# Kernel tuning notes

Measured on AMD Instinct MI355X. Metric: run time of the kernel, lower is better.

Reference implementation:

```python
import jax, jax.numpy as jnp
import numpy as np

N = 50000          # nodes
E = 800000         # edges (before self-loops)
D_IN, D_H, D_OUT = 128, 256, 256
SZ_C = 2           # channels
NUM_GRAPHS = 64
EPS = 1e-6


def setup_inputs() -> dict:
    key = jax.random.key(0)
    ks = jax.random.split(key, 12)
    x = jax.random.normal(ks[0], (N, D_IN), dtype=jnp.float32)
    edge = jax.random.randint(ks[1], (2, E), 0, N, dtype=jnp.int64)
    batch = jnp.sort(jax.random.randint(ks[2], (N,), 0, NUM_GRAPHS, dtype=jnp.int64))
    def glorot(k, shape):
        fan = shape[-2] + shape[-1]
        return jax.random.normal(k, shape, dtype=jnp.float32) * jnp.sqrt(2.0 / fan)
    W0 = glorot(ks[3], (SZ_C, D_IN, D_H)); b0 = jnp.zeros((SZ_C, D_H), jnp.float32)
    W1 = glorot(ks[4], (SZ_C, D_H, D_H));  b1 = jnp.zeros((SZ_C, D_H), jnp.float32)
    W2 = glorot(ks[5], (SZ_C, D_H, D_OUT)); b2 = jnp.zeros((SZ_C, D_OUT), jnp.float32)
    ln_w = jnp.ones((D_OUT,), jnp.float32)
    ln_b = jnp.zeros((D_OUT,), jnp.float32)
    return {"x": x, "edge": edge, "batch": batch,
            "W0": W0, "b0": b0, "W1": W1, "b1": b1, "W2": W2, "b2": b2,
            "ln_w": ln_w, "ln_b": ln_b}


def _gcn_conv(h, W, b, src, dst, norm):
    # PyG GCNConv: linear transform, then deg-normalized scatter-add, then bias
    h = h @ W                                  # [N, d_out]
    msg = h[src] * norm[:, None]               # [E+N, d_out] gathered messages
    agg = jax.ops.segment_sum(msg, dst, num_segments=N)
    return agg + b


def reference(x, edge, batch, W0, b0, W1, b1, W2, b2, ln_w, ln_b):
    # add self-loops (GCNConv default add_self_loops=True)
    loops = jnp.arange(N, dtype=edge.dtype)
    src = jnp.concatenate([edge[0], loops])
    dst = jnp.concatenate([edge[1], loops])
    # symmetric normalization: deg^{-1/2}[src] * deg^{-1/2}[dst], deg over targets
    deg = jax.ops.segment_sum(jnp.ones_like(dst, dtype=x.dtype), dst, num_segments=N)
    dinv = jnp.where(deg > 0, jax.lax.rsqrt(deg), 0.0)
    norm = dinv[src] * dinv[dst]

    channels = []
    for c in range(SZ_C):  # small fixed channel count
        h = x
        for (W, b) in ((W0[c], b0[c]), (W1[c], b1[c]), (W2[c], b2[c])):
            h = _gcn_conv(h, W, b, src, dst, norm)
            h = jax.nn.relu(h) + h  # residual: ReLU output + pre-ReLU input
        channels.append(h)
    channal = jnp.stack(channels)              # [sz_c, N, d_out]

    mean = channal.mean(-1, keepdims=True)
    var = channal.var(-1, keepdims=True)
    out = (channal - mean) * jax.lax.rsqrt(var + EPS) * ln_w + ln_b

    batchs = jnp.ones((SZ_C, 1), channal.dtype) * batch.astype(channal.dtype)[None, :]
    return out, batchs
```

## Files before the change

kernel.cpp:

```cpp
#include <hip/hip_runtime.h>
#include <hip/hip_bf16.h>

typedef __bf16 v8bf __attribute__((ext_vector_type(8)));
typedef float  v4f  __attribute__((ext_vector_type(4)));

constexpr int N_NODES = 50000;
constexpr int N_EDGES = 800000;
constexpr float LN_EPS = 1e-6f;
constexpr int ROW_TILES = N_NODES / 16;

__global__ void probe_kernel(const int* __restrict__ edge, int* __restrict__ flag) {
  int t = threadIdx.x;
  int nz = 0;
  for (int i = t * 2 + 1; i < 4096; i += 128) nz |= (edge[i] != 0);
  unsigned long long m = __ballot(nz);
  if (t == 0) flag[0] = (m == 0ull) ? 1 : 0;
}

__device__ __forceinline__ int ld_idx(const void* base, int i, int is64) {
  int v;
  if (is64) v = (int)((const long long*)base)[(long long)i];
  else      v = ((const int*)base)[i];
  if ((unsigned)v >= (unsigned)N_NODES) v = 0;
  return v;
}


__global__ void init_kernel(int* __restrict__ deg, int* __restrict__ gcount) {
  int i = blockIdx.x * 256 + threadIdx.x;
  if (i < N_NODES) deg[i] = 1;
  if (i == 0) gcount[0] = 0;
}

__global__ void count_kernel(const void* __restrict__ edge, const int* __restrict__ flag,
                             int* __restrict__ deg) {
  int e = blockIdx.x * 256 + threadIdx.x;
  if (e < N_EDGES) atomicAdd(&deg[ld_idx(edge, N_EDGES + e, flag[0])], 1);
}

__global__ __launch_bounds__(256) void block_offsets_kernel(
    const int* __restrict__ deg, int* __restrict__ gcount,
    int* __restrict__ rowstart, int* __restrict__ cursor, float* __restrict__ dinv) {
  __shared__ int ps[256];
  __shared__ int base_s;
  int tid = threadIdx.x;
  int node = blockIdx.x * 256 + tid;
  int d = (node < N_NODES) ? deg[node] : 1;
  int cnt = d - 1;
  ps[tid] = cnt;
  __syncthreads();
#pragma unroll
  for (int off = 1; off < 256; off <<= 1) {
    int v = (tid >= off) ? ps[tid - off] : 0;
    __syncthreads();
    ps[tid] += v;
    __syncthreads();
  }
  if (tid == 255) base_s = atomicAdd(gcount, ps[255]);
  __syncthreads();
  int start = base_s + ps[tid] - cnt;
  if (node < N_NODES) {
    rowstart[node] = start;
    cursor[node]   = start;
    dinv[node]     = rsqrtf((float)max(d, 1));
  }
}

__global__ void scatter_kernel(const void* __restrict__ edge, const int* __restrict__ flag,
                               int* __restrict__ cursor, int* __restrict__ csr_src) {
  int e = blockIdx.x * 256 + threadIdx.x;
  if (e >= N_EDGES) return;
  int f = flag[0];
  int s = ld_idx(edge, e, f);
  int d = ld_idx(edge, N_EDGES + e, f);
  int pos = atomicAdd(&cursor[d], 1);
  if ((unsigned)pos < (unsigned)N_EDGES) csr_src[pos] = s;
}

__global__ void pack_all_kernel(const float* __restrict__ W0, const float* __restrict__ W1,
                                const float* __restrict__ W2, __bf16* __restrict__ Wp) {
  int tid = blockIdx.x * 256 + threadIdx.x;
  const float* src; int local;
  if (tid < 65536)       { src = W0 + (size_t)(tid >> 15) * (128 * 256); local = tid & 32767; }
  else if (tid < 196608) { int t2 = tid - 65536;  src = W1 + (size_t)(t2 >> 16) * 65536; local = t2 & 65535; }
  else                   { int t2 = tid - 196608; src = W2 + (size_t)(t2 >> 16) * 65536; local = t2 & 65535; }
  int j    = local & 7;
  int lane = (local >> 3) & 63;
  int ct   = (local >> 9) & 15;
  int kc   = local >> 13;
  int k    = kc * 32 + ((lane >> 4) << 3) + j;
  int col  = ct * 16 + (lane & 15);
  Wp[tid] = (__bf16)src[k * 256 + col];
}

__global__ __launch_bounds__(256) void prescale_x_kernel(
    const float* __restrict__ x, const float* __restrict__ dinv, __bf16* __restrict__ xd) {
  int t = blockIdx.x * 256 + threadIdx.x;
  int node = t >> 4;
  int d0 = (t & 15) * 8;
  float di = dinv[node];
  v4f f0 = *(const v4f*)(x + (size_t)node * 128 + d0);
  v4f f1 = *(const v4f*)(x + (size_t)node * 128 + d0 + 4);
  v8bf o;
#pragma unroll
  for (int j = 0; j < 4; j++) { o[j] = (__bf16)(di * f0[j]); o[4 + j] = (__bf16)(di * f1[j]); }
  *(v8bf*)(xd + (size_t)node * 128 + d0) = o;
}

__global__ __launch_bounds__(256) void agg128_kernel(
    const __bf16* __restrict__ Yd, const int* __restrict__ rowstart,
    const int* __restrict__ deg, const int* __restrict__ csr_src,
    const float* __restrict__ dinv, __bf16* __restrict__ U) {
  int node = blockIdx.x * 4 + (threadIdx.x >> 6);
  int lane = threadIdx.x & 63;
  int sub = lane >> 4;
  int d0 = (lane & 15) * 8;

  int start = rowstart[node];
  int cnt = deg[node] - 1;
  start = max(0, min(start, N_EDGES));
  cnt = max(0, min(cnt, N_EDGES - start));
  int e = start, end = start + cnt;

  float di = dinv[node];
  v8bf ys = *(const v8bf*)(Yd + (unsigned)(node * 128 + d0));

  float a[8];
#pragma unroll
  for (int j = 0; j < 8; j++) a[j] = 0.f;

  for (; e + 16 <= end; e += 16) {
    int s0 = csr_src[e + sub];
    int s1 = csr_src[e + 4 + sub];
    int s2 = csr_src[e + 8 + sub];
    int s3 = csr_src[e + 12 + sub];
    if ((unsigned)s0 >= (unsigned)N_NODES) s0 = 0;
    if ((unsigned)s1 >= (unsigned)N_NODES) s1 = 0;
    if ((unsigned)s2 >= (unsigned)N_NODES) s2 = 0;
    if ((unsigned)s3 >= (unsigned)N_NODES) s3 = 0;
    v8bf y0 = *(const v8bf*)(Yd + (unsigned)(s0 * 128 + d0));
    v8bf y1 = *(const v8bf*)(Yd + (unsigned)(s1 * 128 + d0));
    v8bf y2 = *(const v8bf*)(Yd + (unsigned)(s2 * 128 + d0));
    v8bf y3 = *(const v8bf*)(Yd + (unsigned)(s3 * 128 + d0));
#pragma unroll
    for (int j = 0; j < 8; j++)
      a[j] += ((float)y0[j] + (float)y1[j]) + ((float)y2[j] + (float)y3[j]);
  }
  if (e + 8 <= end) {
    int s0 = csr_src[e + sub];
    int s1 = csr_src[e + 4 + sub];
    if ((unsigned)s0 >= (unsigned)N_NODES) s0 = 0;
    if ((unsigned)s1 >= (unsigned)N_NODES) s1 = 0;
    v8bf y0 = *(const v8bf*)(Yd + (unsigned)(s0 * 128 + d0));
    v8bf y1 = *(const v8bf*)(Yd + (unsigned)(s1 * 128 + d0));
#pragma unroll
    for (int j = 0; j < 8; j++) a[j] += (float)y0[j] + (float)y1[j];
    e += 8;
  }
  if (e + 4 <= end) {
    int s0 = csr_src[e + sub];
    if ((unsigned)s0 >= (unsigned)N_NODES) s0 = 0;
    v8bf y0 = *(const v8bf*)(Yd + (unsigned)(s0 * 128 + d0));
#pragma unroll
    for (int j = 0; j < 8; j++) a[j] += (float)y0[j];
    e += 4;
  }
  int rem = end - e;
  if (sub < rem) {
    int s0 = csr_src[e + sub];
    if ((unsigned)s0 >= (unsigned)N_NODES) s0 = 0;
    v8bf y0 = *(const v8bf*)(Yd + (unsigned)(s0 * 128 + d0));
#pragma unroll
    for (int j = 0; j < 8; j++) a[j] += (float)y0[j];
  }

#pragma unroll
  for (int off = 16; off < 64; off <<= 1)
#pragma unroll
    for (int j = 0; j < 8; j++) a[j] += __shfl_xor(a[j], off);

  if (sub == 0) {
    v8bf u;
#pragma unroll
    for (int j = 0; j < 8; j++) u[j] = (__bf16)(di * (a[j] + (float)ys[j]));
    *(v8bf*)(U + (unsigned)(node * 128 + d0)) = u;
  }
}

__global__ __launch_bounds__(256) void agg_fused512_kernel(
    const __bf16* __restrict__ A,
    const int* __restrict__ rowstart, const int* __restrict__ deg,
    const int* __restrict__ csr_src, const float* __restrict__ dinv,
    __bf16* __restrict__ U) {
  int node = blockIdx.x * 4 + (threadIdx.x >> 6);
  int lane = threadIdx.x & 63;
  int d0 = lane * 8;

  int start = rowstart[node];
  int cnt = deg[node] - 1;
  start = max(0, min(start, N_EDGES));
  cnt = max(0, min(cnt, N_EDGES - start));
  int e = start, end = start + cnt;

  float di = dinv[node];
  v8bf ys = *(const v8bf*)(A + (unsigned)(node * 512 + d0));

  float a[8];
#pragma unroll
  for (int j = 0; j < 8; j++) a[j] = 0.f;

  for (; e + 8 <= end; e += 8) {
    int s0 = csr_src[e],     s1 = csr_src[e + 1];
    int s2 = csr_src[e + 2], s3 = csr_src[e + 3];
    int s4 = csr_src[e + 4], s5 = csr_src[e + 5];
    int s6 = csr_src[e + 6], s7 = csr_src[e + 7];
    if ((unsigned)s0 >= (unsigned)N_NODES) s0 = 0;
    if ((unsigned)s1 >= (unsigned)N_NODES) s1 = 0;
    if ((unsigned)s2 >= (unsigned)N_NODES) s2 = 0;
    if ((unsigned)s3 >= (unsigned)N_NODES) s3 = 0;
    if ((unsigned)s4 >= (unsigned)N_NODES) s4 = 0;
    if ((unsigned)s5 >= (unsigned)N_NODES) s5 = 0;
    if ((unsigned)s6 >= (unsigned)N_NODES) s6 = 0;
    if ((unsigned)s7 >= (unsigned)N_NODES) s7 = 0;
    v8bf y0 = *(const v8bf*)(A + (unsigned)(s0 * 512 + d0));
    v8bf y1 = *(const v8bf*)(A + (unsigned)(s1 * 512 + d0));
    v8bf y2 = *(const v8bf*)(A + (unsigned)(s2 * 512 + d0));
    v8bf y3 = *(const v8bf*)(A + (unsigned)(s3 * 512 + d0));
    v8bf y4 = *(const v8bf*)(A + (unsigned)(s4 * 512 + d0));
    v8bf y5 = *(const v8bf*)(A + (unsigned)(s5 * 512 + d0));
    v8bf y6 = *(const v8bf*)(A + (unsigned)(s6 * 512 + d0));
    v8bf y7 = *(const v8bf*)(A + (unsigned)(s7 * 512 + d0));
#pragma unroll
    for (int j = 0; j < 8; j++)
      a[j] += (((float)y0[j] + (float)y1[j]) + ((float)y2[j] + (float)y3[j])) +
              (((float)y4[j] + (float)y5[j]) + ((float)y6[j] + (float)y7[j]));
  }
  if (e + 4 <= end) {
    int s0 = csr_src[e],     s1 = csr_src[e + 1];
    int s2 = csr_src[e + 2], s3 = csr_src[e + 3];
    if ((unsigned)s0 >= (unsigned)N_NODES) s0 = 0;
    if ((unsigned)s1 >= (unsigned)N_NODES) s1 = 0;
    if ((unsigned)s2 >= (unsigned)N_NODES) s2 = 0;
    if ((unsigned)s3 >= (unsigned)N_NODES) s3 = 0;
    v8bf y0 = *(const v8bf*)(A + (unsigned)(s0 * 512 + d0));
    v8bf y1 = *(const v8bf*)(A + (unsigned)(s1 * 512 + d0));
    v8bf y2 = *(const v8bf*)(A + (unsigned)(s2 * 512 + d0));
    v8bf y3 = *(const v8bf*)(A + (unsigned)(s3 * 512 + d0));
#pragma unroll
    for (int j = 0; j < 8; j++)
      a[j] += ((float)y0[j] + (float)y1[j]) + ((float)y2[j] + (float)y3[j]);
    e += 4;
  }
  for (; e < end; e++) {
    int s0 = csr_src[e];
    if ((unsigned)s0 >= (unsigned)N_NODES) s0 = 0;
    v8bf y0 = *(const v8bf*)(A + (unsigned)(s0 * 512 + d0));
#pragma unroll
    for (int j = 0; j < 8; j++) a[j] += (float)y0[j];
  }

  v8bf u;
#pragma unroll
  for (int j = 0; j < 8; j++) u[j] = (__bf16)(di * (a[j] + (float)ys[j]));
  *(v8bf*)(U + (unsigned)(node * 512 + d0)) = u;
}

template <int K, int LDA, int LDO>
__global__ __launch_bounds__(256, 2) void gemm_mid_kernel(
    const __bf16* __restrict__ A, const __bf16* __restrict__ Wp,
    const float* __restrict__ bias, const float* __restrict__ dinv,
    __bf16* __restrict__ Hd) {
  constexpr int KC = K / 32;
  int lane = threadIdx.x & 63;
  int wave = threadIdx.x >> 6;

  v8bf bfrag[KC][4];
#pragma unroll
  for (int kc = 0; kc < KC; kc++)
#pragma unroll
    for (int c4 = 0; c4 < 4; c4++)
      bfrag[kc][c4] = *(const v8bf*)(Wp + ((size_t)((kc * 16 + wave * 4 + c4) * 64 + lane)) * 8);

  int arow = lane & 15;
  int akq = (lane >> 4) * 8;
  int ccol = wave * 64 + (lane & 15);
  float bcol[4];
#pragma unroll
  for (int c4 = 0; c4 < 4; c4++) bcol[c4] = bias[ccol + c4 * 16];

  for (int t = blockIdx.x; t < ROW_TILES; t += gridDim.x) {
    int row0 = t * 16;
    const __bf16* Ap = A + (size_t)(row0 + arow) * LDA + akq;
    v8bf af[KC];
#pragma unroll
    for (int kc = 0; kc < KC; kc++) af[kc] = *(const v8bf*)(Ap + kc * 32);

    v4f acc[4];
#pragma unroll
    for (int c4 = 0; c4 < 4; c4++) acc[c4] = (v4f){0.f, 0.f, 0.f, 0.f};
#pragma unroll
    for (int kc = 0; kc < KC; kc++)
#pragma unroll
      for (int c4 = 0; c4 < 4; c4++)
        acc[c4] = __builtin_amdgcn_mfma_f32_16x16x32_bf16(af[kc], bfrag[kc][c4], acc[c4], 0, 0, 0);

    int crow = row0 + ((lane >> 4) << 2);
    float dv[4];
#pragma unroll
    for (int r = 0; r < 4; r++) dv[r] = dinv[crow + r];
#pragma unroll
    for (int c4 = 0; c4 < 4; c4++)
#pragma unroll
      for (int r = 0; r < 4; r++) {
        float z = acc[c4][r] + bcol[c4];
        float h = z + fmaxf(z, 0.f);
        Hd[(size_t)(crow + r) * LDO + ccol + c4 * 16] = (__bf16)(dv[r] * h);
      }
  }
}

__global__ __launch_bounds__(256, 2) void gemm_final_kernel(
    const __bf16* __restrict__ A, const __bf16* __restrict__ Wp,
    const float* __restrict__ bias, const float* __restrict__ lnw,
    const float* __restrict__ lnb, float* __restrict__ out) {
  constexpr int KC = 8;
  constexpr int LDA = 512;
  __shared__ float ls1[4][16];
  __shared__ float ls2[4][16];
  int lane = threadIdx.x & 63;
  int wave = threadIdx.x >> 6;

  v8bf bfrag[KC][4];
#pragma unroll
  for (int kc = 0; kc < KC; kc++)
#pragma unroll
    for (int c4 = 0; c4 < 4; c4++)
      bfrag[kc][c4] = *(const v8bf*)(Wp + ((size_t)((kc * 16 + wave * 4 + c4) * 64 + lane)) * 8);

  int arow = lane & 15;
  int akq = (lane >> 4) * 8;
  int g = lane >> 4;
  int ccol = wave * 64 + (lane & 15);
  float bcol[4], wcol[4], lbcol[4];
#pragma unroll
  for (int c4 = 0; c4 < 4; c4++) {
    int col = ccol + c4 * 16;
    bcol[c4] = bias[col];
    wcol[c4] = lnw[col];
    lbcol[c4] = lnb[col];
  }

  for (int t = blockIdx.x; t < ROW_TILES; t += gridDim.x) {
    int row0 = t * 16;
    const __bf16* Ap = A + (size_t)(row0 + arow) * LDA + akq;
    v8bf af[KC];
#pragma unroll
    for (int kc = 0; kc < KC; kc++) af[kc] = *(const v8bf*)(Ap + kc * 32);

    v4f acc[4];
#pragma unroll
    for (int c4 = 0; c4 < 4; c4++) acc[c4] = (v4f){0.f, 0.f, 0.f, 0.f};
#pragma unroll
    for (int kc = 0; kc < KC; kc++)
#pragma unroll
      for (int c4 = 0; c4 < 4; c4++)
        acc[c4] = __builtin_amdgcn_mfma_f32_16x16x32_bf16(af[kc], bfrag[kc][c4], acc[c4], 0, 0, 0);

    float h[4][4];
#pragma unroll
    for (int c4 = 0; c4 < 4; c4++)
#pragma unroll
      for (int r = 0; r < 4; r++) {
        float z = acc[c4][r] + bcol[c4];
        h[c4][r] = z + fmaxf(z, 0.f);
      }

    float s1[4], s2[4];
#pragma unroll
    for (int r = 0; r < 4; r++) {
      s1[r] = 0.f; s2[r] = 0.f;
#pragma unroll
      for (int c4 = 0; c4 < 4; c4++) { s1[r] += h[c4][r]; s2[r] += h[c4][r] * h[c4][r]; }
    }
#pragma unroll
    for (int off = 1; off < 16; off <<= 1)
#pragma unroll
      for (int r = 0; r < 4; r++) {
        s1[r] += __shfl_xor(s1[r], off);
        s2[r] += __shfl_xor(s2[r], off);
      }
    if ((lane & 15) == 0) {
#pragma unroll
      for (int r = 0; r < 4; r++) { ls1[wave][g * 4 + r] = s1[r]; ls2[wave][g * 4 + r] = s2[r]; }
    }
    __syncthreads();
#pragma unroll
    for (int r = 0; r < 4; r++) {
      int row = g * 4 + r;
      float t1 = ls1[0][row] + ls1[1][row] + ls1[2][row] + ls1[3][row];
      float t2 = ls2[0][row] + ls2[1][row] + ls2[2][row] + ls2[3][row];
      float mean = t1 * (1.0f / 256.0f);
      float var = t2 * (1.0f / 256.0f) - mean * mean;
      float rstd = rsqrtf(fmaxf(var, 0.f) + LN_EPS);
#pragma unroll
      for (int c4 = 0; c4 < 4; c4++)
        out[(size_t)(row0 + row) * 256 + ccol + c4 * 16] =
            (h[c4][r] - mean) * rstd * wcol[c4] + lbcol[c4];
    }
    __syncthreads();
  }
}

__global__ void batchs_kernel(const void* __restrict__ batch, const int* __restrict__ flag,
                              float* __restrict__ ob) {
  int i = blockIdx.x * 256 + threadIdx.x;
  if (i >= N_NODES) return;
  int f = flag[0];
  int v;
  if (f) v = (int)((const long long*)batch)[i];
  else   v = ((const int*)batch)[i];
  float b = (float)v;
  ob[i] = b;
  ob[N_NODES + i] = b;
}


extern "C" void kernel_launch(void* const* d_in, const int* in_sizes, int n_in,
                              void* d_out, int out_size, void* d_ws, size_t ws_size,
                              hipStream_t stream) {
  const float* x    = (const float*)d_in[0];
  const void*  edge = d_in[1];
  const void*  batch= d_in[2];
  const float* W0   = (const float*)d_in[3];
  const float* b0   = (const float*)d_in[4];
  const float* W1   = (const float*)d_in[5];
  const float* b1   = (const float*)d_in[6];
  const float* W2   = (const float*)d_in[7];
  const float* b2   = (const float*)d_in[8];
  const float* lnw  = (const float*)d_in[9];
  const float* lnb  = (const float*)d_in[10];

  float* out_x = (float*)d_out;
  float* out_b = (float*)d_out + (size_t)2 * N_NODES * 256;

  __bf16* UC  = (__bf16*)out_x;
  __bf16* HdC = (__bf16*)(out_x + (size_t)N_NODES * 256);

  char* p = (char*)d_ws;
  __bf16* Ubuf  = (__bf16*)p;  p += (size_t)N_NODES * 256 * 2;
  __bf16* xd    = Ubuf;
  __bf16* U0    = Ubuf + (size_t)N_NODES * 128;
  int* csr_src  = (int*)p;     p += (size_t)N_EDGES * 4;
  int* deg      = (int*)p;     p += (size_t)N_NODES * 4;
  int* cursor   = (int*)p;     p += (size_t)N_NODES * 4;
  int* rowstart = (int*)p;     p += (size_t)N_NODES * 4;
  float* dinv   = (float*)p;   p += (size_t)N_NODES * 4;
  int* flag     = (int*)p;     p += 16;
  int* gcount   = (int*)p;     p += 16;
  __bf16* Wp    = (__bf16*)p;

  const int EB = (N_EDGES + 255) / 256;
  const int NB = (N_NODES + 255) / 256;

  probe_kernel<<<1, 64, 0, stream>>>((const int*)edge, flag);
  init_kernel<<<NB, 256, 0, stream>>>(deg, gcount);
  count_kernel<<<EB, 256, 0, stream>>>(edge, flag, deg);
  block_offsets_kernel<<<NB, 256, 0, stream>>>(deg, gcount, rowstart, cursor, dinv);
  scatter_kernel<<<EB, 256, 0, stream>>>(edge, flag, cursor, csr_src);

  pack_all_kernel<<<1280, 256, 0, stream>>>(W0, W1, W2, Wp);

  prescale_x_kernel<<<3125, 256, 0, stream>>>(x, dinv, xd);
  agg128_kernel<<<N_NODES / 4, 256, 0, stream>>>(xd, rowstart, deg, csr_src, dinv, U0);

  gemm_mid_kernel<128, 128, 512><<<512, 256, 0, stream>>>(U0, Wp, b0, dinv, HdC);
  gemm_mid_kernel<128, 128, 512><<<512, 256, 0, stream>>>(U0, Wp + 32768, b0 + 256, dinv,
                                                          HdC + 256);

  agg_fused512_kernel<<<N_NODES / 4, 256, 0, stream>>>(HdC, rowstart, deg, csr_src, dinv, UC);
  gemm_mid_kernel<256, 512, 512><<<512, 256, 0, stream>>>(UC, Wp + 65536, b1, dinv, HdC);
  gemm_mid_kernel<256, 512, 512><<<512, 256, 0, stream>>>(UC + 256, Wp + 131072, b1 + 256,
                                                          dinv, HdC + 256);

  agg_fused512_kernel<<<N_NODES / 4, 256, 0, stream>>>(HdC, rowstart, deg, csr_src, dinv, UC);
  gemm_final_kernel<<<512, 256, 0, stream>>>(UC + 256, Wp + 262144, b2 + 256, lnw, lnb,
                                             out_x + (size_t)N_NODES * 256);
  gemm_final_kernel<<<512, 256, 0, stream>>>(UC, Wp + 196608, b2, lnw, lnb, out_x);

  batchs_kernel<<<NB, 256, 0, stream>>>(batch, flag, out_b);
}
```

Before: 622.4 us.

## Fuse neighbor aggregation with following GEMM for first two GCN layers

Replaces the separate aggregation and dual-channel GEMM kernels of layers 0 and 1 with fused kernels. Each block aggregates 16 nodes into an XOR-swizzled LDS tile, then runs MFMA for both channels and writes the prescaled residual-ReLU output directly. This removes the global write and reread of the aggregated intermediate and four launches. In exchange, each block streams the full weight fragments from L2 rather than keeping them in registers across a persistent loop. The output buffers are also re-aliased and the final GEMM launch order swapped to match.

After: 595.4 us. 1.05x faster.

```diff
diff --git a/kernel.cpp b/kernel.cpp
--- a/kernel.cpp
+++ b/kernel.cpp
@@ -107,91 +107,268 @@
   *(v8bf*)(xd + (size_t)node * 128 + d0) = o;
 }
 
-__global__ __launch_bounds__(256) void agg128_kernel(
+__global__ __launch_bounds__(256) void fused0_kernel(
     const __bf16* __restrict__ Yd, const int* __restrict__ rowstart,
     const int* __restrict__ deg, const int* __restrict__ csr_src,
-    const float* __restrict__ dinv, __bf16* __restrict__ U) {
-  int node = blockIdx.x * 4 + (threadIdx.x >> 6);
+    const float* __restrict__ dinv, const __bf16* __restrict__ Wp,
+    const float* __restrict__ bias,
+    __bf16* __restrict__ Hd) {
+  __shared__ __bf16 lds[16 * 128];
+  char* lb = (char*)lds;
+  int wave = threadIdx.x >> 6;
   int lane = threadIdx.x & 63;
   int sub = lane >> 4;
-  int d0 = (lane & 15) * 8;
-
-  int start = rowstart[node];
-  int cnt = deg[node] - 1;
-  start = max(0, min(start, N_EDGES));
-  cnt = max(0, min(cnt, N_EDGES - start));
-  int e = start, end = start + cnt;
-
-  float di = dinv[node];
-  v8bf ys = *(const v8bf*)(Yd + (unsigned)(node * 128 + d0));
-
-  float a[8];
-#pragma unroll
-  for (int j = 0; j < 8; j++) a[j] = 0.f;
-
-  for (; e + 16 <= end; e += 16) {
-    int s0 = csr_src[e + sub];
-    int s1 = csr_src[e + 4 + sub];
-    int s2 = csr_src[e + 8 + sub];
-    int s3 = csr_src[e + 12 + sub];
-    if ((unsigned)s0 >= (unsigned)N_NODES) s0 = 0;
-    if ((unsigned)s1 >= (unsigned)N_NODES) s1 = 0;
-    if ((unsigned)s2 >= (unsigned)N_NODES) s2 = 0;
-    if ((unsigned)s3 >= (unsigned)N_NODES) s3 = 0;
-    v8bf y0 = *(const v8bf*)(Yd + (unsigned)(s0 * 128 + d0));
-    v8bf y1 = *(const v8bf*)(Yd + (unsigned)(s1 * 128 + d0));
-    v8bf y2 = *(const v8bf*)(Yd + (unsigned)(s2 * 128 + d0));
-    v8bf y3 = *(const v8bf*)(Yd + (unsigned)(s3 * 128 + d0));
-#pragma unroll
-    for (int j = 0; j < 8; j++)
-      a[j] += ((float)y0[j] + (float)y1[j]) + ((float)y2[j] + (float)y3[j]);
-  }
-  if (e + 8 <= end) {
-    int s0 = csr_src[e + sub];
-    int s1 = csr_src[e + 4 + sub];
-    if ((unsigned)s0 >= (unsigned)N_NODES) s0 = 0;
-    if ((unsigned)s1 >= (unsigned)N_NODES) s1 = 0;
-    v8bf y0 = *(const v8bf*)(Yd + (unsigned)(s0 * 128 + d0));
-    v8bf y1 = *(const v8bf*)(Yd + (unsigned)(s1 * 128 + d0));
-#pragma unroll
-    for (int j = 0; j < 8; j++) a[j] += (float)y0[j] + (float)y1[j];
-    e += 8;
-  }
-  if (e + 4 <= end) {
-    int s0 = csr_src[e + sub];
-    if ((unsigned)s0 >= (unsigned)N_NODES) s0 = 0;
-    v8bf y0 = *(const v8bf*)(Yd + (unsigned)(s0 * 128 + d0));
-#pragma unroll
-    for (int j = 0; j < 8; j++) a[j] += (float)y0[j];
-    e += 4;
-  }
-  int rem = end - e;
-  if (sub < rem) {
-    int s0 = csr_src[e + sub];
-    if ((unsigned)s0 >= (unsigned)N_NODES) s0 = 0;
-    v8bf y0 = *(const v8bf*)(Yd + (unsigned)(s0 * 128 + d0));
-#pragma unroll
-    for (int j = 0; j < 8; j++) a[j] += (float)y0[j];
-  }
-
-#pragma unroll
-  for (int off = 16; off < 64; off <<= 1)
-#pragma unroll
-    for (int j = 0; j < 8; j++) a[j] += __shfl_xor(a[j], off);
-
-  if (sub == 0) {
-    v8bf u;
-#pragma unroll
-    for (int j = 0; j < 8; j++) u[j] = (__bf16)(di * (a[j] + (float)ys[j]));
-    *(v8bf*)(U + (unsigned)(node * 128 + d0)) = u;
-  }
-}
-
-__global__ __launch_bounds__(256) void agg_fused512_kernel(
+  int dc = (lane & 15) * 8;
+
+  for (int i = 0; i < 4; i++) {
+    int row = wave * 4 + i;
+    int node = blockIdx.x * 16 + row;
+
+    int start = rowstart[node];
+    int cnt = deg[node] - 1;
+    start = max(0, min(start, N_EDGES));
+    cnt = max(0, min(cnt, N_EDGES - start));
+    int e = start, end = start + cnt;
+
+    float di = dinv[node];
+    v8bf ys = *(const v8bf*)(Yd + (unsigned)(node * 128 + dc));
+
+    float a[8];
+#pragma unroll
+    for (int j = 0; j < 8; j++) a[j] = 0.f;
+
+    for (; e + 16 <= end; e += 16) {
+      int s0 = csr_src[e + sub];
+      int s1 = csr_src[e + 4 + sub];
+      int s2 = csr_src[e + 8 + sub];
+      int s3 = csr_src[e + 12 + sub];
+      if ((unsigned)s0 >= (unsigned)N_NODES) s0 = 0;
+      if ((unsigned)s1 >= (unsigned)N_NODES) s1 = 0;
+      if ((unsigned)s2 >= (unsigned)N_NODES) s2 = 0;
+      if ((unsigned)s3 >= (unsigned)N_NODES) s3 = 0;
+      v8bf y0 = *(const v8bf*)(Yd + (unsigned)(s0 * 128 + dc));
+      v8bf y1 = *(const v8bf*)(Yd + (unsigned)(s1 * 128 + dc));
+      v8bf y2 = *(const v8bf*)(Yd + (unsigned)(s2 * 128 + dc));
+      v8bf y3 = *(const v8bf*)(Yd + (unsigned)(s3 * 128 + dc));
+#pragma unroll
+      for (int j = 0; j < 8; j++)
+        a[j] += ((float)y0[j] + (float)y1[j]) + ((float)y2[j] + (float)y3[j]);
+    }
+    if (e + 8 <= end) {
+      int s0 = csr_src[e + sub];
+      int s1 = csr_src[e + 4 + sub];
+      if ((unsigned)s0 >= (unsigned)N_NODES) s0 = 0;
+      if ((unsigned)s1 >= (unsigned)N_NODES) s1 = 0;
+      v8bf y0 = *(const v8bf*)(Yd + (unsigned)(s0 * 128 + dc));
+      v8bf y1 = *(const v8bf*)(Yd + (unsigned)(s1 * 128 + dc));
+#pragma unroll
+      for (int j = 0; j < 8; j++) a[j] += (float)y0[j] + (float)y1[j];
+      e += 8;
+    }
+    if (e + 4 <= end) {
+      int s0 = csr_src[e + sub];
+      if ((unsigned)s0 >= (unsigned)N_NODES) s0 = 0;
+      v8bf y0 = *(const v8bf*)(Yd + (unsigned)(s0 * 128 + dc));
+#pragma unroll
+      for (int j = 0; j < 8; j++) a[j] += (float)y0[j];
+      e += 4;
+    }
+    int rem = end - e;
+    if (sub < rem) {
+      int s0 = csr_src[e + sub];
+      if ((unsigned)s0 >= (unsigned)N_NODES) s0 = 0;
+      v8bf y0 = *(const v8bf*)(Yd + (unsigned)(s0 * 128 + dc));
+#pragma unroll
+      for (int j = 0; j < 8; j++) a[j] += (float)y0[j];
+    }
+
+#pragma unroll
+    for (int off = 16; off < 64; off <<= 1)
+#pragma unroll
+      for (int j = 0; j < 8; j++) a[j] += __shfl_xor(a[j], off);
+
+    if (sub == 0) {
+      v8bf u;
+#pragma unroll
+      for (int j = 0; j < 8; j++) u[j] = (__bf16)(di * (a[j] + (float)ys[j]));
+      int byte = (row * 256 + dc * 2) ^ ((row & 7) << 4);
+      *(v8bf*)(lb + byte) = u;
+    }
+  }
+  __syncthreads();
+
+  int ch = wave >> 1, q = wave & 1;
+  const __bf16* Wsec = Wp + ch * 32768;
+  const float* bch = bias + ch * 256;
+  int arow = lane & 15;
+  int g = lane >> 4;
+
+  v8bf af[4];
+#pragma unroll
+  for (int kc = 0; kc < 4; kc++) {
+    int byte = (arow * 256 + g * 16 + kc * 64) ^ ((arow & 7) << 4);
+    af[kc] = *(const v8bf*)(lb + byte);
+  }
+
+  int crow = blockIdx.x * 16 + (g << 2);
+  float dv[4];
+#pragma unroll
+  for (int r = 0; r < 4; r++) dv[r] = dinv[crow + r];
+
+#pragma unroll
+  for (int c4 = 0; c4 < 8; c4++) {
+    int ct = q * 8 + c4;
+    v8bf bf[4];
+#pragma unroll
+    for (int kc = 0; kc < 4; kc++)
+      bf[kc] = *(const v8bf*)(Wsec + (size_t)((kc * 16 + ct) * 64 + lane) * 8);
+    v4f acc = (v4f){0.f, 0.f, 0.f, 0.f};
+#pragma unroll
+    for (int kc = 0; kc < 4; kc++)
+      acc = __builtin_amdgcn_mfma_f32_16x16x32_bf16(af[kc], bf[kc], acc, 0, 0, 0);
+    int wcol = ct * 16 + (lane & 15);
+    float bb = bch[wcol];
+#pragma unroll
+    for (int r = 0; r < 4; r++) {
+      float z = acc[r] + bb;
+      float h = z + fmaxf(z, 0.f);
+      Hd[(size_t)(crow + r) * 512 + ch * 256 + wcol] = (__bf16)(dv[r] * h);
+    }
+  }
+}
+
+__global__ __launch_bounds__(256) void fusedA_kernel(
     const __bf16* __restrict__ A,
     const int* __restrict__ rowstart, const int* __restrict__ deg,
     const int* __restrict__ csr_src, const float* __restrict__ dinv,
-    __bf16* __restrict__ U) {
+    const __bf16* __restrict__ Wp,
+    const float* __restrict__ bias,
+    __bf16* __restrict__ Hd) {
+  __shared__ __bf16 lds[16 * 512];
+  char* lb = (char*)lds;
+  int wave = threadIdx.x >> 6;
+  int lane = threadIdx.x & 63;
+  int d0 = lane * 8;
+
+  for (int i = 0; i < 4; i++) {
+    int row = wave * 4 + i;
+    int node = blockIdx.x * 16 + row;
+
+    int start = rowstart[node];
+    int cnt = deg[node] - 1;
+    start = max(0, min(start, N_EDGES));
+    cnt = max(0, min(cnt, N_EDGES - start));
+    int e = start, end = start + cnt;
+
+    float di = dinv[node];
+    v8bf ys = *(const v8bf*)(A + (unsigned)(node * 512 + d0));
+
+    float a[8];
+#pragma unroll
+    for (int j = 0; j < 8; j++) a[j] = 0.f;
+
+    for (; e + 8 <= end; e += 8) {
+      int s0 = csr_src[e],     s1 = csr_src[e + 1];
+      int s2 = csr_src[e + 2], s3 = csr_src[e + 3];
+      int s4 = csr_src[e + 4], s5 = csr_src[e + 5];
+      int s6 = csr_src[e + 6], s7 = csr_src[e + 7];
+      if ((unsigned)s0 >= (unsigned)N_NODES) s0 = 0;
+      if ((unsigned)s1 >= (unsigned)N_NODES) s1 = 0;
+      if ((unsigned)s2 >= (unsigned)N_NODES) s2 = 0;
+      if ((unsigned)s3 >= (unsigned)N_NODES) s3 = 0;
+      if ((unsigned)s4 >= (unsigned)N_NODES) s4 = 0;
+      if ((unsigned)s5 >= (unsigned)N_NODES) s5 = 0;
+      if ((unsigned)s6 >= (unsigned)N_NODES) s6 = 0;
+      if ((unsigned)s7 >= (unsigned)N_NODES) s7 = 0;
+      v8bf y0 = *(const v8bf*)(A + (unsigned)(s0 * 512 + d0));
+      v8bf y1 = *(const v8bf*)(A + (unsigned)(s1 * 512 + d0));
+      v8bf y2 = *(const v8bf*)(A + (unsigned)(s2 * 512 + d0));
+      v8bf y3 = *(const v8bf*)(A + (unsigned)(s3 * 512 + d0));
+      v8bf y4 = *(const v8bf*)(A + (unsigned)(s4 * 512 + d0));
+      v8bf y5 = *(const v8bf*)(A + (unsigned)(s5 * 512 + d0));
+      v8bf y6 = *(const v8bf*)(A + (unsigned)(s6 * 512 + d0));
+      v8bf y7 = *(const v8bf*)(A + (unsigned)(s7 * 512 + d0));
+#pragma unroll
+      for (int j = 0; j < 8; j++)
+        a[j] += (((float)y0[j] + (float)y1[j]) + ((float)y2[j] + (float)y3[j])) +
+                (((float)y4[j] + (float)y5[j]) + ((float)y6[j] + (float)y7[j]));
+    }
+    if (e + 4 <= end) {
+      int s0 = csr_src[e],     s1 = csr_src[e + 1];
+      int s2 = csr_src[e + 2], s3 = csr_src[e + 3];
+      if ((unsigned)s0 >= (unsigned)N_NODES) s0 = 0;
+      if ((unsigned)s1 >= (unsigned)N_NODES) s1 = 0;
+      if ((unsigned)s2 >= (unsigned)N_NODES) s2 = 0;
+      if ((unsigned)s3 >= (unsigned)N_NODES) s3 = 0;
+      v8bf y0 = *(const v8bf*)(A + (unsigned)(s0 * 512 + d0));
+      v8bf y1 = *(const v8bf*)(A + (unsigned)(s1 * 512 + d0));
+      v8bf y2 = *(const v8bf*)(A + (unsigned)(s2 * 512 + d0));
+      v8bf y3 = *(const v8bf*)(A + (unsigned)(s3 * 512 + d0));
+#pragma unroll
+      for (int j = 0; j < 8; j++)
+        a[j] += ((float)y0[j] + (float)y1[j]) + ((float)y2[j] + (float)y3[j]);
+      e += 4;
+    }
+    for (; e < end; e++) {
+      int s0 = csr_src[e];
+      if ((unsigned)s0 >= (unsigned)N_NODES) s0 = 0;
+      v8bf y0 = *(const v8bf*)(A + (unsigned)(s0 * 512 + d0));
+#pragma unroll
+      for (int j = 0; j < 8; j++) a[j] += (float)y0[j];
+    }
+
+    v8bf u;
+#pragma unroll
+    for (int j = 0; j < 8; j++) u[j] = (__bf16)(di * (a[j] + (float)ys[j]));
+    int byte = (row * 1024 + lane * 16) ^ ((row & 7) << 4);
+    *(v8bf*)(lb + byte) = u;
+  }
+  __syncthreads();
+
+  int ch = wave >> 1, q = wave & 1;
+  const __bf16* Wsec = Wp + ch * 65536;
+  const float* bch = bias + ch * 256;
+  int arow = lane & 15;
+  int g = lane >> 4;
+
+  v8bf af[8];
+#pragma unroll
+  for (int kc = 0; kc < 8; kc++) {
+    int byte = (arow * 1024 + ch * 512 + g * 16 + kc * 64) ^ ((arow & 7) << 4);
+    af[kc] = *(const v8bf*)(lb + byte);
+  }
+
+  int crow = blockIdx.x * 16 + (g << 2);
+  float dv[4];
+#pragma unroll
+  for (int r = 0; r < 4; r++) dv[r] = dinv[crow + r];
+
+#pragma unroll
+  for (int c4 = 0; c4 < 8; c4++) {
+    int ct = q * 8 + c4;
+    v8bf bf[8];
+#pragma unroll
+    for (int kc = 0; kc < 8; kc++)
+      bf[kc] = *(const v8bf*)(Wsec + (size_t)((kc * 16 + ct) * 64 + lane) * 8);
+    v4f acc = (v4f){0.f, 0.f, 0.f, 0.f};
+#pragma unroll
+    for (int kc = 0; kc < 8; kc++)
+      acc = __builtin_amdgcn_mfma_f32_16x16x32_bf16(af[kc], bf[kc], acc, 0, 0, 0);
+    int wcol = ct * 16 + (lane & 15);
+    float bb = bch[wcol];
+#pragma unroll
+    for (int r = 0; r < 4; r++) {
+      float z = acc[r] + bb;
+      float h = z + fmaxf(z, 0.f);
+      Hd[(size_t)(crow + r) * 512 + ch * 256 + wcol] = (__bf16)(dv[r] * h);
+    }
+  }
+}
+
+__global__ __launch_bounds__(256) void agg_fused512_kernel(
+    const __bf16* __restrict__ A, const int* __restrict__ rowstart,
+    const int* __restrict__ deg, const int* __restrict__ csr_src,
+    const float* __restrict__ dinv, __bf16* __restrict__ U) {
   int node = blockIdx.x * 4 + (threadIdx.x >> 6);
   int lane = threadIdx.x & 63;
   int d0 = lane * 8;
@@ -265,60 +442,6 @@
   *(v8bf*)(U + (unsigned)(node * 512 + d0)) = u;
 }
 
-template <int K, int LDA, int LDO>
-__global__ __launch_bounds__(256, 2) void gemm_mid_kernel(
-    const __bf16* __restrict__ A, const __bf16* __restrict__ Wp,
-    const float* __restrict__ bias, const float* __restrict__ dinv,
-    __bf16* __restrict__ Hd) {
-  constexpr int KC = K / 32;
-  int lane = threadIdx.x & 63;
-  int wave = threadIdx.x >> 6;
-
-  v8bf bfrag[KC][4];
-#pragma unroll
-  for (int kc = 0; kc < KC; kc++)
-#pragma unroll
-    for (int c4 = 0; c4 < 4; c4++)
-      bfrag[kc][c4] = *(const v8bf*)(Wp + ((size_t)((kc * 16 + wave * 4 + c4) * 64 + lane)) * 8);
-
-  int arow = lane & 15;
-  int akq = (lane >> 4) * 8;
-  int ccol = wave * 64 + (lane & 15);
-  float bcol[4];
-#pragma unroll
-  for (int c4 = 0; c4 < 4; c4++) bcol[c4] = bias[ccol + c4 * 16];
-
-  for (int t = blockIdx.x; t < ROW_TILES; t += gridDim.x) {
-    int row0 = t * 16;
-    const __bf16* Ap = A + (size_t)(row0 + arow) * LDA + akq;
-    v8bf af[KC];
-#pragma unroll
-    for (int kc = 0; kc < KC; kc++) af[kc] = *(const v8bf*)(Ap + kc * 32);
-
-    v4f acc[4];
-#pragma unroll
-    for (int c4 = 0; c4 < 4; c4++) acc[c4] = (v4f){0.f, 0.f, 0.f, 0.f};
-#pragma unroll
-    for (int kc = 0; kc < KC; kc++)
-#pragma unroll
-      for (int c4 = 0; c4 < 4; c4++)
-        acc[c4] = __builtin_amdgcn_mfma_f32_16x16x32_bf16(af[kc], bfrag[kc][c4], acc[c4], 0, 0, 0);
-
-    int crow = row0 + ((lane >> 4) << 2);
-    float dv[4];
-#pragma unroll
-    for (int r = 0; r < 4; r++) dv[r] = dinv[crow + r];
-#pragma unroll
-    for (int c4 = 0; c4 < 4; c4++)
-#pragma unroll
-      for (int r = 0; r < 4; r++) {
-        float z = acc[c4][r] + bcol[c4];
-        float h = z + fmaxf(z, 0.f);
-        Hd[(size_t)(crow + r) * LDO + ccol + c4 * 16] = (__bf16)(dv[r] * h);
-      }
-  }
-}
-
 __global__ __launch_bounds__(256, 2) void gemm_final_kernel(
     const __bf16* __restrict__ A, const __bf16* __restrict__ Wp,
     const float* __restrict__ bias, const float* __restrict__ lnw,
@@ -443,13 +566,12 @@
   float* out_x = (float*)d_out;
   float* out_b = (float*)d_out + (size_t)2 * N_NODES * 256;
 
-  __bf16* UC  = (__bf16*)out_x;
-  __bf16* HdC = (__bf16*)(out_x + (size_t)N_NODES * 256);
+  __bf16* H2 = (__bf16*)out_x;
+  __bf16* H1 = (__bf16*)(out_x + (size_t)N_NODES * 256);
+  __bf16* UC = H1;
 
   char* p = (char*)d_ws;
-  __bf16* Ubuf  = (__bf16*)p;  p += (size_t)N_NODES * 256 * 2;
-  __bf16* xd    = Ubuf;
-  __bf16* U0    = Ubuf + (size_t)N_NODES * 128;
+  __bf16* xd    = (__bf16*)p;  p += (size_t)N_NODES * 256 * 2;
   int* csr_src  = (int*)p;     p += (size_t)N_EDGES * 4;
   int* deg      = (int*)p;     p += (size_t)N_NODES * 4;
   int* cursor   = (int*)p;     p += (size_t)N_NODES * 4;
@@ -469,23 +591,16 @@
   scatter_kernel<<<EB, 256, 0, stream>>>(edge, flag, cursor, csr_src);
 
   pack_all_kernel<<<1280, 256, 0, stream>>>(W0, W1, W2, Wp);
-
   prescale_x_kernel<<<3125, 256, 0, stream>>>(x, dinv, xd);
-  agg128_kernel<<<N_NODES / 4, 256, 0, stream>>>(xd, rowstart, deg, csr_src, dinv, U0);
-
-  gemm_mid_kernel<128, 128, 512><<<512, 256, 0, stream>>>(U0, Wp, b0, dinv, HdC);
-  gemm_mid_kernel<128, 128, 512><<<512, 256, 0, stream>>>(U0, Wp + 32768, b0 + 256, dinv,
-                                                          HdC + 256);
-
-  agg_fused512_kernel<<<N_NODES / 4, 256, 0, stream>>>(HdC, rowstart, deg, csr_src, dinv, UC);
-  gemm_mid_kernel<256, 512, 512><<<512, 256, 0, stream>>>(UC, Wp + 65536, b1, dinv, HdC);
-  gemm_mid_kernel<256, 512, 512><<<512, 256, 0, stream>>>(UC + 256, Wp + 131072, b1 + 256,
-                                                          dinv, HdC + 256);
-
-  agg_fused512_kernel<<<N_NODES / 4, 256, 0, stream>>>(HdC, rowstart, deg, csr_src, dinv, UC);
+
+  fused0_kernel<<<ROW_TILES, 256, 0, stream>>>(xd, rowstart, deg, csr_src, dinv,
+                                               Wp, b0, H1);
+  fusedA_kernel<<<ROW_TILES, 256, 0, stream>>>(H1, rowstart, deg, csr_src, dinv,
+                                               Wp + 65536, b1, H2);
+  agg_fused512_kernel<<<N_NODES / 4, 256, 0, stream>>>(H2, rowstart, deg, csr_src, dinv, UC);
+  gemm_final_kernel<<<512, 256, 0, stream>>>(UC, Wp + 196608, b2, lnw, lnb, out_x);
   gemm_final_kernel<<<512, 256, 0, stream>>>(UC + 256, Wp + 262144, b2 + 256, lnw, lnb,
                                              out_x + (size_t)N_NODES * 256);
-  gemm_final_kernel<<<512, 256, 0, stream>>>(UC, Wp + 196608, b2, lnw, lnb, out_x);
 
   batchs_kernel<<<NB, 256, 0, stream>>>(batch, flag, out_b);
 }
```
